# Optimization experiments

Measured on AMD Instinct MI355X. Metric: run time of the kernel, lower is better.

The kernel has to match this reference:

```python
import jax, jax.numpy as jnp
import numpy as np

N_ITERS = 32
AO_SCALE = 4.0


def _cross_blur(rx):
    # ReplicationPad2d(1) + conv2d with fixed cross filter [[0,.25,0],[.25,0,.25],[0,.25,0]]
    p = jnp.pad(rx, ((0, 0), (0, 0), (1, 1), (1, 1)), mode='edge')
    return 0.25 * (p[:, :, :-2, 1:-1] + p[:, :, 2:, 1:-1]
                   + p[:, :, 1:-1, :-2] + p[:, :, 1:-1, 2:])


def _height_to_ao(x):
    # 32 sequential pad+stencil iterations (simplistic_height_to_AO)
    rx = jax.lax.fori_loop(0, N_ITERS, lambda i, r: _cross_blur(r), x)
    return 1.0 - jnp.clip((rx - x) * AO_SCALE, 0.0, 1.0)


def setup_inputs() -> dict:
    key = jax.random.key(0)
    k1, k2 = jax.random.split(key)
    x = jax.random.uniform(k1, (1, 1, 4096, 4096), dtype=jnp.float32)       # heightmap
    normals = jax.random.normal(k2, (1, 3, 4096, 4096), dtype=jnp.float32)  # surface normals
    return {"x": x, "normals": normals}


def reference(x, normals):
    # forward slices x to 1 channel; here x already has 1 channel
    ao = _height_to_ao(x)  # [B,1,H,W]
    # normals_to_diffuse_render: dot with light dir ld1, clamp at 0, remap, modulate by AO
    ld1 = jnp.array([0.7053, -0.7053, 0.7053], dtype=jnp.float32).reshape(1, 3, 1, 1)
    d1 = jnp.sum(normals * ld1, axis=1, keepdims=True)  # [B,1,H,W]
    d1 = jnp.maximum(d1, 0.0)
    diffuse = d1 * 0.3 + 0.7
    return diffuse * ao
```

## Files before the change

kernel.cpp:

```cpp
#include <hip/hip_runtime.h>

#define N 4096
#define B 32
#define SST 66
#define OST 34
#define SROWS 69

__device__ constexpr float BIN32[33] = {
    1.f, 32.f, 496.f, 4960.f, 35960.f, 201376.f, 906192.f, 3365856.f,
    10518300.f, 28048800.f, 64512240.f, 129024480.f, 225792840.f,
    347373600.f, 471435600.f, 565722720.f, 601080390.f, 565722720.f,
    471435600.f, 347373600.f, 225792840.f, 129024480.f, 64512240.f,
    28048800.f, 10518300.f, 3365856.f, 906192.f, 201376.f, 35960.f,
    4960.f, 496.f, 32.f, 1.f};

__device__ __forceinline__ int mir(int c) {
    c = (c < 0) ? (-1 - c) : c;
    return (c >= N) ? (2 * N - 1 - c) : c;
}

__device__ __forceinline__ unsigned short f2bf(float x) {
    unsigned b = __float_as_uint(x);
    b += 0x7FFFu + ((b >> 16) & 1u);
    return (unsigned short)(b >> 16);
}
__device__ __forceinline__ float bf2f(unsigned short u) {
    return __uint_as_float(((unsigned)u) << 16);
}

__device__ __forceinline__ size_t strip_off(int tx, int ty) {
    long e = (tx >= 4080) ? ((long)(ty + 16) * 32 + (tx - 4080))
                          : (132096L + (long)(ty - 4080) * (long)N + (tx + 16));
    return (size_t)(64 + e / 4064) * N + (size_t)(e % 4064);
}

__device__ __forceinline__ float4 shade2(float4 v, float4 h, float4 df) {
    const float SC = 0x1p-64f;
    float4 o;
    o.x = df.x * (1.0f - fminf(fmaxf((v.x * SC - h.x) * 4.0f, 0.0f), 1.0f));
    o.y = df.y * (1.0f - fminf(fmaxf((v.y * SC - h.y) * 4.0f, 0.0f), 1.0f));
    o.z = df.z * (1.0f - fminf(fmaxf((v.z * SC - h.z) * 4.0f, 0.0f), 1.0f));
    o.w = df.w * (1.0f - fminf(fmaxf((v.w * SC - h.w) * 4.0f, 0.0f), 1.0f));
    return o;
}

__device__ __forceinline__ void conv33(const float* __restrict__ S, int rowAddr, float acc[8]) {
#pragma unroll
    for (int i = 0; i < 8; ++i) acc[i] = 0.f;
    {
        float w[24];
#pragma unroll
        for (int j = 0; j < 12; ++j)
            *(float2*)&w[2 * j] = *(const float2*)&S[rowAddr + 2 * j];
#pragma unroll
        for (int k = 0; k < 16; ++k) {
            const float c = BIN32[k];
#pragma unroll
            for (int i = 0; i < 8; ++i) acc[i] = fmaf(c, w[i + k], acc[i]);
        }
    }
    {
        float w[24];
#pragma unroll
        for (int j = 0; j < 12; ++j)
            *(float2*)&w[2 * j] = *(const float2*)&S[rowAddr + 16 + 2 * j];
#pragma unroll
        for (int k = 16; k <= 32; ++k) {
            const float c = BIN32[k];
#pragma unroll
            for (int i = 0; i < 8; ++i) acc[i] = fmaf(c, w[i + k - 16], acc[i]);
        }
    }
}

__global__ __launch_bounds__(256, 8) void p1_antidiag(const float* __restrict__ src,
                                                      unsigned short* __restrict__ tcore,
                                                      float* __restrict__ tstrip,
                                                      const float* __restrict__ nrm,
                                                      unsigned short* __restrict__ dif) {
    __shared__ float S[SROWS * SST + 8];
    const int bx = blockIdx.x, by = blockIdx.y;
    const int X0 = 32 * bx - 16, Y0 = 32 * by - 16;
    const bool edgeT = (bx == 0) | (by == 0) | (bx == 128) | (by == 128);
    const int tid = (int)threadIdx.x;

    for (int m = tid; m < 64 * 16; m += 256) {
        const int ly = m >> 4, lx4 = m & 15;
        const int lyp = ly - 16, lxp = 4 * lx4 - 16;
        float4 v;
        if (!edgeT) {
            v = *(const float4*)(src + (size_t)(Y0 + lyp) * N + (X0 + lxp));
        } else {
            const float* row = src + (size_t)mir(Y0 + lyp) * N;
            v = make_float4(row[mir(X0 + lxp)], row[mir(X0 + lxp + 1)],
                            row[mir(X0 + lxp + 2)], row[mir(X0 + lxp + 3)]);
        }
        const int r0 = lxp + lyp;
        if (r0 >= -3 && r0 <= 62) {
            const int base = (r0 + 3) * SST + (lxp + 16);
            S[base]                 = v.x;
            S[base + (SST + 1)]     = v.y;
            S[base + 2 * (SST + 1)] = v.z;
            S[base + 3 * (SST + 1)] = v.w;
        }
    }
    __syncthreads();

    const int d = tid >> 2, h = tid & 3;
    const int lo = max(0, d - 31), hi = min(31, d);
    const int L = (lo & ~3) + 8 * h;
    const bool act = (d <= 62) && (L <= hi);
    float acc[8];
    if (act) conv33(S, (d + 3) * SST + L, acc);
    __syncthreads();

    float* SO = S;
    if (act) {
#pragma unroll
        for (int i = 0; i < 8; ++i) {
            const int lx = L + i;
            if (lx >= lo && lx <= hi) SO[(d - lx) * OST + lx] = acc[i];
        }
    }
    __syncthreads();

    {
        const int ly = tid >> 3, lx4 = tid & 7;
        const float2 v01 = *(const float2*)&SO[ly * OST + 4 * lx4];
        const float2 v23 = *(const float2*)&SO[ly * OST + 4 * lx4 + 2];
        const int wcol = X0 + 4 * lx4 + 16;
        const int wrow = Y0 + ly + 16;
        if (wcol < N && wrow < N) {
            ushort4 u;
            u.x = f2bf(v01.x); u.y = f2bf(v01.y); u.z = f2bf(v23.x); u.w = f2bf(v23.y);
            *(ushort4*)(tcore + (size_t)wrow * N + wcol) = u;
        } else {
            const int ty = Y0 + ly;
            const float vv[4] = {v01.x, v01.y, v23.x, v23.y};
#pragma unroll
            for (int e = 0; e < 4; ++e) {
                const int tx = X0 + 4 * lx4 + e;
                tstrip[strip_off(tx, ty)] = vv[e];
            }
        }
    }

    if (bx < 128 && by < 128) {
        const int ly = tid >> 3, lx4 = tid & 7;
        const size_t dbase = (size_t)(32 * by + ly) * N + 32 * bx + 4 * lx4;
        const float L0 = 0.7053f, L1 = -0.7053f, L2 = 0.7053f;
        const float4 n0 = *(const float4*)(nrm + dbase);
        const float4 n1 = *(const float4*)(nrm + (size_t)N * N + dbase);
        const float4 n2 = *(const float4*)(nrm + 2 * (size_t)N * N + dbase);
        ushort4 u;
        u.x = f2bf(fmaxf(n0.x * L0 + n1.x * L1 + n2.x * L2, 0.0f) * 0.3f + 0.7f);
        u.y = f2bf(fmaxf(n0.y * L0 + n1.y * L1 + n2.y * L2, 0.0f) * 0.3f + 0.7f);
        u.z = f2bf(fmaxf(n0.z * L0 + n1.z * L1 + n2.z * L2, 0.0f) * 0.3f + 0.7f);
        u.w = f2bf(fmaxf(n0.w * L0 + n1.w * L1 + n2.w * L2, 0.0f) * 0.3f + 0.7f);
        *(ushort4*)(dif + dbase) = u;
    }
}

template <int STRIPS>
__global__ __launch_bounds__(256, 8) void p2_diag(const unsigned short* __restrict__ tcore,
                                                  const float* __restrict__ tstrip,
                                                  float* __restrict__ dst,
                                                  const float* __restrict__ xin,
                                                  const unsigned short* __restrict__ dif) {
    __shared__ float S[SROWS * SST + 8];
    int X0, Y0;
    if constexpr (STRIPS) {
        if (blockIdx.y == 0) { X0 = 4064; Y0 = 32 * (int)blockIdx.x; }
        else                 { X0 = 32 * (int)blockIdx.x; Y0 = 4064; }
    } else {
        X0 = 32 * (int)blockIdx.x; Y0 = 32 * (int)blockIdx.y;
    }
    const int tid = (int)threadIdx.x;

    for (int m = tid; m < 64 * 16; m += 256) {
        const int ly = m >> 4, lx4 = m & 15;
        const int lyp = ly - 16, lxp = 4 * lx4 - 16;
        float4 v;
        if constexpr (!STRIPS) {
            const ushort4 u = *(const ushort4*)(tcore + (size_t)(Y0 + lyp + 16) * N + (X0 + lxp + 16));
            v = make_float4(bf2f(u.x), bf2f(u.y), bf2f(u.z), bf2f(u.w));
        } else {
            const int ty = Y0 + lyp;
            float tmp[4];
#pragma unroll
            for (int e = 0; e < 4; ++e) {
                const int tx = X0 + lxp + e;
                tmp[e] = (tx < 4080 && ty < 4080)
                             ? bf2f(tcore[(size_t)(ty + 16) * N + (tx + 16)])
                             : tstrip[strip_off(tx, ty)];
            }
            v = make_float4(tmp[0], tmp[1], tmp[2], tmp[3]);
        }
        const int r0 = lxp - lyp + 31;
        if (r0 >= -3 && r0 <= 62) {
            const int base = (r0 + 3) * SST + (lxp + 16);
            S[base]                 = v.x;
            S[base + (SST + 1)]     = v.y;
            S[base + 2 * (SST + 1)] = v.z;
            S[base + 3 * (SST + 1)] = v.w;
        }
    }
    __syncthreads();

    const int d = tid >> 2, h = tid & 3;
    const int lo = max(0, d - 31), hi = min(31, d);
    const int L = (lo & ~3) + 8 * h;
    const bool act = (d <= 62) && (L <= hi);
    float acc[8];
    if (act) conv33(S, (d + 3) * SST + L, acc);
    __syncthreads();

    float* SO = S;
    if (act) {
#pragma unroll
        for (int i = 0; i < 8; ++i) {
            const int lx = L + i;
            if (lx >= lo && lx <= hi) SO[(lx - d + 31) * OST + lx] = acc[i];
        }
    }
    __syncthreads();

    {
        const int ly = tid >> 3, lx4 = tid & 7;
        const float2 v01 = *(const float2*)&SO[ly * OST + 4 * lx4];
        const float2 v23 = *(const float2*)&SO[ly * OST + 4 * lx4 + 2];
        const float4 v = make_float4(v01.x, v01.y, v23.x, v23.y);
        const size_t base = (size_t)(Y0 + ly) * N + X0 + 4 * lx4;
        const float4 h4 = *(const float4*)(xin + base);
        const ushort4 ud = *(const ushort4*)(dif + base);
        const float4 df = make_float4(bf2f(ud.x), bf2f(ud.y), bf2f(ud.z), bf2f(ud.w));
        *(float4*)(dst + base) = shade2(v, h4, df);
    }
}

extern "C" void kernel_launch(void* const* d_in, const int* in_sizes, int n_in,
                              void* d_out, int out_size, void* d_ws, size_t ws_size,
                              hipStream_t stream) {
    const float* x       = (const float*)d_in[0];
    const float* normals = (const float*)d_in[1];
    float* out = (float*)d_out;
    unsigned short* ws16 = (unsigned short*)d_ws;
    unsigned short* dif  = ws16 + (size_t)N * N;

    dim3 block(256);

    p1_antidiag<<<dim3(129, 129), block, 0, stream>>>(x, ws16, out, normals, dif);
    p2_diag<1><<<dim3(128, 2), block, 0, stream>>>(ws16, out, out, x, dif);
    p2_diag<0><<<dim3(127, 127), block, 0, stream>>>(ws16, out, out, x, dif);
}
```

Baseline: 138.3 us.

## Split diffuse computation into dedicated interleaved blocks within fused first-pass grid

Stops computing the diffuse term inside each stencil tile block. A 1D grid is launched instead, where every ninth block is a dedicated grid-stride worker that computes diffuse over the whole image and the rest run the stencil tiles. The goal is to shorten the stencil blocks and let the memory-bound normals streaming overlap with the compute-heavy stencil work. The cost is heterogeneous blocks, plus extra index math and a less tile-local access pattern.

```diff
diff --git a/kernel.cpp b/kernel.cpp
--- a/kernel.cpp
+++ b/kernel.cpp
@@ -5,6 +5,9 @@
 #define SST 66
 #define OST 34
 #define SROWS 69
+#define NP1 16641
+#define NDIF 2081
+#define NTOT 18729
 
 __device__ constexpr float BIN32[33] = {
     1.f, 32.f, 496.f, 4960.f, 35960.f, 201376.f, 906192.f, 3365856.f,
@@ -73,16 +76,39 @@
     }
 }
 
-__global__ __launch_bounds__(256, 8) void p1_antidiag(const float* __restrict__ src,
-                                                      unsigned short* __restrict__ tcore,
-                                                      float* __restrict__ tstrip,
-                                                      const float* __restrict__ nrm,
-                                                      unsigned short* __restrict__ dif) {
+__global__ __launch_bounds__(256, 8) void p1_fused(const float* __restrict__ src,
+                                                   unsigned short* __restrict__ tcore,
+                                                   float* __restrict__ tstrip,
+                                                   const float* __restrict__ nrm,
+                                                   unsigned short* __restrict__ dif) {
     __shared__ float S[SROWS * SST + 8];
-    const int bx = blockIdx.x, by = blockIdx.y;
+    const int bid = (int)blockIdx.x;
+    const int tid = (int)threadIdx.x;
+
+    if ((bid % 9) == 8) {
+        const int difid = bid / 9;
+        const float L0 = 0.7053f, L1 = -0.7053f, L2 = 0.7053f;
+        const size_t NN = (size_t)N * N;
+        for (size_t i = (size_t)difid * 256 + tid; i < NN / 4; i += (size_t)NDIF * 256) {
+            const size_t base = 4 * i;
+            const float4 n0 = *(const float4*)(nrm + base);
+            const float4 n1 = *(const float4*)(nrm + NN + base);
+            const float4 n2 = *(const float4*)(nrm + 2 * NN + base);
+            ushort4 u;
+            u.x = f2bf(fmaxf(n0.x * L0 + n1.x * L1 + n2.x * L2, 0.0f) * 0.3f + 0.7f);
+            u.y = f2bf(fmaxf(n0.y * L0 + n1.y * L1 + n2.y * L2, 0.0f) * 0.3f + 0.7f);
+            u.z = f2bf(fmaxf(n0.z * L0 + n1.z * L1 + n2.z * L2, 0.0f) * 0.3f + 0.7f);
+            u.w = f2bf(fmaxf(n0.w * L0 + n1.w * L1 + n2.w * L2, 0.0f) * 0.3f + 0.7f);
+            *(ushort4*)(dif + base) = u;
+        }
+        return;
+    }
+
+    const int p1idx = (bid / 9) * 8 + (bid % 9);
+    if (p1idx >= NP1) return;
+    const int bx = p1idx % 129, by = p1idx / 129;
     const int X0 = 32 * bx - 16, Y0 = 32 * by - 16;
     const bool edgeT = (bx == 0) | (by == 0) | (bx == 128) | (by == 128);
-    const int tid = (int)threadIdx.x;
 
     for (int m = tid; m < 64 * 16; m += 256) {
         const int ly = m >> 4, lx4 = m & 15;
@@ -143,21 +169,6 @@
                 tstrip[strip_off(tx, ty)] = vv[e];
             }
         }
-    }
-
-    if (bx < 128 && by < 128) {
-        const int ly = tid >> 3, lx4 = tid & 7;
-        const size_t dbase = (size_t)(32 * by + ly) * N + 32 * bx + 4 * lx4;
-        const float L0 = 0.7053f, L1 = -0.7053f, L2 = 0.7053f;
-        const float4 n0 = *(const float4*)(nrm + dbase);
-        const float4 n1 = *(const float4*)(nrm + (size_t)N * N + dbase);
-        const float4 n2 = *(const float4*)(nrm + 2 * (size_t)N * N + dbase);
-        ushort4 u;
-        u.x = f2bf(fmaxf(n0.x * L0 + n1.x * L1 + n2.x * L2, 0.0f) * 0.3f + 0.7f);
-        u.y = f2bf(fmaxf(n0.y * L0 + n1.y * L1 + n2.y * L2, 0.0f) * 0.3f + 0.7f);
-        u.z = f2bf(fmaxf(n0.z * L0 + n1.z * L1 + n2.z * L2, 0.0f) * 0.3f + 0.7f);
-        u.w = f2bf(fmaxf(n0.w * L0 + n1.w * L1 + n2.w * L2, 0.0f) * 0.3f + 0.7f);
-        *(ushort4*)(dif + dbase) = u;
     }
 }
 
@@ -249,7 +260,7 @@
 
     dim3 block(256);
 
-    p1_antidiag<<<dim3(129, 129), block, 0, stream>>>(x, ws16, out, normals, dif);
+    p1_fused<<<dim3(NTOT), block, 0, stream>>>(x, ws16, out, normals, dif);
     p2_diag<1><<<dim3(128, 2), block, 0, stream>>>(ws16, out, out, x, dif);
     p2_diag<0><<<dim3(127, 127), block, 0, stream>>>(ws16, out, out, x, dif);
 }
```

After: 144.7 us. +4.6%, slower.
